# Optimization experiments

Measured on AMD Instinct MI355X. Metric: run time of the kernel, lower is better.

## Reference

```python
import jax, jax.numpy as jnp
import numpy as np

EPS = 1e-5
TOP_K = 2


def _dwconv3x3(x, w):
    # depthwise 3x3, stride 1, padding 1 (SAME)
    return jax.lax.conv_general_dilated(
        x, w, window_strides=(1, 1), padding='SAME',
        feature_group_count=x.shape[1],
        dimension_numbers=('NCHW', 'OIHW', 'NCHW'))


def _bn(x, g, b, m, v):
    # inference-mode BatchNorm2d
    s = g / jnp.sqrt(v + EPS)
    return x * s[None, :, None, None] + (b - m * s)[None, :, None, None]


def setup_inputs() -> dict:
    key = jax.random.key(0)
    ks = jax.random.split(key, 26)
    Bsz, D, H = 16, 384, 32
    S, E, HID = 64, 8, 768
    n, u = jax.random.normal, jax.random.uniform
    inp = {}
    inp['x'] = n(ks[0], (Bsz, D, H, H), jnp.float32)
    inp['dw1_w'] = n(ks[1], (D, 1, 3, 3)) * 0.1
    inp['bn1_g'] = u(ks[2], (D,), minval=0.5, maxval=1.5)
    inp['bn1_b'] = n(ks[3], (D,)) * 0.1
    inp['bn1_m'] = n(ks[4], (D,)) * 0.1
    inp['bn1_v'] = u(ks[5], (D,), minval=0.5, maxval=1.5)
    inp['dw2_w'] = n(ks[6], (D, 1, 3, 3)) * 0.1
    inp['bn2_g'] = u(ks[7], (D,), minval=0.5, maxval=1.5)
    inp['bn2_b'] = n(ks[8], (D,)) * 0.1
    inp['bn2_m'] = n(ks[9], (D,)) * 0.1
    inp['bn2_v'] = u(ks[10], (D,), minval=0.5, maxval=1.5)
    inp['ln_w'] = u(ks[11], (D,), minval=0.5, maxval=1.5)
    inp['ln_b'] = n(ks[12], (D,)) * 0.1
    inp['bcdt_w'] = n(ks[13], (3 * S, D)) * 0.02
    inp['dws_w'] = n(ks[14], (3 * S, 1, 3, 3)) * 0.1
    inp['hproj_w'] = n(ks[15], (D, D)) * 0.02
    inp['A'] = u(ks[16], (S,), minval=1.0, maxval=16.0)
    inp['gate_w'] = n(ks[17], (E, D)) * 0.02
    inp['gate_b'] = n(ks[18], (E,)) * 0.02
    inp['w1'] = n(ks[19], (E, HID, D)) * 0.02
    inp['b1'] = n(ks[20], (E, HID)) * 0.02
    inp['w2'] = n(ks[21], (E, D, HID)) * 0.02
    inp['b2'] = n(ks[22], (E, D)) * 0.02
    inp['w3'] = n(ks[23], (E, HID, D)) * 0.02
    inp['b3'] = n(ks[24], (E, HID)) * 0.02
    return inp


def reference(x, dw1_w, bn1_g, bn1_b, bn1_m, bn1_v, dw2_w, bn2_g, bn2_b, bn2_m,
              bn2_v, ln_w, ln_b, bcdt_w, dws_w, hproj_w, A, gate_w, gate_b,
              w1, b1, w2, b2, w3, b3):
    Bsz, D, H, W = x.shape
    L = H * W
    S = A.shape[0]
    E = gate_w.shape[0]
    # x = x + dwconv1(x)
    x = x + _bn(_dwconv3x3(x, dw1_w), bn1_g, bn1_b, bn1_m, bn1_v)
    x_prev = x
    # LayerNorm1D over channel dim of (B, C, L)
    xf = x.reshape(Bsz, D, L)
    mu = xf.mean(axis=1, keepdims=True)
    var = xf.var(axis=1, keepdims=True)
    xn = (xf - mu) / jnp.sqrt(var + EPS) * ln_w[None, :, None] + ln_b[None, :, None]
    # Slim_SSD mixer
    bcdt = jnp.einsum('cd,bdl->bcl', bcdt_w, xn)            # 1x1 conv1d
    bcdt = _dwconv3x3(bcdt.reshape(Bsz, 3 * S, H, W), dws_w).reshape(Bsz, 3 * S, L)
    Bm, Cm, dt = jnp.split(bcdt, 3, axis=1)                  # each (B, S, L)
    Am = jax.nn.softmax(dt + A[None, :, None], axis=-1)      # softmax over L
    h = jnp.einsum('bdl,bsl->bds', xn, Am * Bm)              # (B, D, S)
    h = jax.nn.silu(jnp.einsum('ed,bds->bes', hproj_w, h))   # h_proj + SiLU
    y = jnp.einsum('bes,bsl->bel', h, Cm).reshape(Bsz, D, H, W)
    x = x_prev + y
    # x = x + dwconv2(x)
    x = x + _bn(_dwconv3x3(x, dw2_w), bn2_g, bn2_b, bn2_m, bn2_v)
    # SparseMoE (TopkRouter, eval mode, filter_radio=0 -> mask==1, bias buffer==0)
    t = x.transpose(0, 2, 3, 1).reshape(-1, D)               # (N, D) tokens
    N = t.shape[0]
    logits = t @ gate_w.T + gate_b                           # (N, E)
    vals, idx = jax.lax.top_k(logits, TOP_K)
    probs = jax.nn.softmax(vals, axis=1)                     # softmax over top-k logits
    wfull = jnp.zeros((N, E), t.dtype).at[jnp.arange(N)[:, None], idx].set(probs)
    ymoe = jnp.zeros_like(t)
    for e in range(E):
        he = jax.nn.silu(t @ w1[e].T + b1[e]) * (t @ w3[e].T + b3[e])
        ymoe = ymoe + (he @ w2[e].T + b2[e]) * wfull[:, e:e + 1]
    x = x + ymoe.reshape(Bsz, H, W, D).transpose(0, 3, 1, 2)
    # dropout is identity in eval mode
    return (x, h)
```

## Files before the change

### kernel.cpp

```cpp
#include <hip/hip_runtime.h>
#include <hip/hip_bf16.h>

#define BSZ 16
#define DCH 384
#define LSP 1024
#define SST 64
#define NEXP 8
#define HID 768
#define NTOK 16384
#define MOE_MAXT 520

#define OFF_X1    0ULL
#define OFF_XN    25165824ULL
#define OFF_BCDT  50331648ULL
#define OFF_BCDTC 62914560ULL
#define OFF_H     75497472ULL
#define OFF_X2    77070336ULL
#define OFF_META  102236160ULL
#define OFF_LOGITS (OFF_META)
#define OFF_PROBS  (OFF_META +  524288ULL)
#define OFF_IDX    (OFF_META +  655360ULL)
#define OFF_CNT    (OFF_META +  786432ULL)
#define OFF_FILL   (OFF_META +  786464ULL)
#define OFF_OFFS   (OFF_META +  786496ULL)
#define OFF_TOFF   (OFF_META +  786560ULL)
#define OFF_LTOK   (OFF_META +  786624ULL)
#define OFF_LP     (OFF_META +  917696ULL)
#define OFF_TPOS   (OFF_META + 1048768ULL)
#define OFF_HE    0ULL
#define OFF_T16   OFF_BCDT
#define OFF_W1B   OFF_BCDTC
#define OFF_W3B   (OFF_BCDTC + 4718592ULL)
#define OFF_W2B   (OFF_BCDTC + 9437184ULL)
#define OFF_YMOE  OFF_X2
#define OFF_HPRE  OFF_X2

typedef __attribute__((ext_vector_type(8))) short bf16x8;
typedef __attribute__((ext_vector_type(4))) float f32x4;
typedef __attribute__((ext_vector_type(4))) unsigned short u16x4;

__device__ __forceinline__ unsigned short f2bf(float f) {
  union { float f; unsigned int u; } x; x.f = f;
  unsigned int r = (x.u + 0x7fffu + ((x.u >> 16) & 1u)) >> 16;
  return (unsigned short)r;
}
__device__ __forceinline__ float bf2f(unsigned short s) {
  union { unsigned int u; float f; } x; x.u = ((unsigned int)s) << 16; return x.f;
}

__device__ __forceinline__ void async16(const void* g, void* l) {
  unsigned long long gi = reinterpret_cast<unsigned long long>(g);
  unsigned int li = (unsigned int)reinterpret_cast<unsigned long long>(l);
  __builtin_amdgcn_global_load_lds(
      (const __attribute__((address_space(1))) unsigned int*)gi,
      (__attribute__((address_space(3))) unsigned int*)(unsigned long long)li,
      16, 0, 0);
}

__global__ void k_dwbnres(const float* __restrict__ x, const float* __restrict__ w,
                          const float* __restrict__ g, const float* __restrict__ bb,
                          const float* __restrict__ mm, const float* __restrict__ vv,
                          float* __restrict__ out, int C) {
  int bc = blockIdx.x;
  int c = bc % C;
  __shared__ float tile[34 * 34];
  const float* img = x + (size_t)bc * 1024;
  for (int i = threadIdx.x; i < 34 * 34; i += 256) tile[i] = 0.f;
  __syncthreads();
  for (int i = threadIdx.x; i < 1024; i += 256) {
    int r = i >> 5, cc = i & 31;
    tile[(r + 1) * 34 + (cc + 1)] = img[i];
  }
  __syncthreads();
  float w0 = w[c*9+0], w1 = w[c*9+1], w2 = w[c*9+2], w3 = w[c*9+3], w4 = w[c*9+4],
        w5 = w[c*9+5], w6 = w[c*9+6], w7 = w[c*9+7], w8 = w[c*9+8];
  bool res = (g != nullptr);
  float scale = 1.f, bias = 0.f;
  if (res) { float s = g[c] * rsqrtf(vv[c] + 1e-5f); scale = s; bias = bb[c] - mm[c] * s; }
  for (int i = threadIdx.x; i < 1024; i += 256) {
    int r = i >> 5, cc = i & 31;
    const float* t0 = &tile[r * 34 + cc];
    float acc = t0[0]*w0 + t0[1]*w1 + t0[2]*w2
              + t0[34]*w3 + t0[35]*w4 + t0[36]*w5
              + t0[68]*w6 + t0[69]*w7 + t0[70]*w8;
    float o = res ? (t0[35] + acc * scale + bias) : acc;
    out[(size_t)bc * 1024 + i] = o;
  }
}

__global__ void k_layernorm(const float* __restrict__ x, const float* __restrict__ lw,
                            const float* __restrict__ lb, float* __restrict__ xn) {
  int lane = threadIdx.x & 63;
  int slice = threadIdx.x >> 6;
  int pos0 = blockIdx.x * 64;
  int b = pos0 >> 10;
  int l = (pos0 & 1023) + lane;
  const float* xb = x + (size_t)b * DCH * LSP + l;
  float s = 0.f, s2 = 0.f;
  for (int d = slice * 96; d < slice * 96 + 96; d++) {
    float v = xb[(size_t)d * LSP];
    s += v; s2 += v * v;
  }
  __shared__ float red[2][4][64];
  red[0][slice][lane] = s; red[1][slice][lane] = s2;
  __syncthreads();
  if (slice == 0) {
    s  = red[0][0][lane] + red[0][1][lane] + red[0][2][lane] + red[0][3][lane];
    s2 = red[1][0][lane] + red[1][1][lane] + red[1][2][lane] + red[1][3][lane];
    float mu = s * (1.f / 384.f);
    float var = s2 * (1.f / 384.f) - mu * mu;
    red[0][0][lane] = mu;
    red[1][0][lane] = rsqrtf(var + 1e-5f);
  }
  __syncthreads();
  float mu = red[0][0][lane], rs = red[1][0][lane];
  float* xnb = xn + (size_t)b * DCH * LSP + l;
  for (int d = slice * 96; d < slice * 96 + 96; d++) {
    float v = xb[(size_t)d * LSP];
    xnb[(size_t)d * LSP] = (v - mu) * rs * lw[d] + lb[d];
  }
}

__global__ void k_bcdt(const float* __restrict__ xn, const float* __restrict__ wt,
                       float* __restrict__ out) {
  int lt = blockIdx.x, ct = blockIdx.y, b = blockIdx.z;
  __shared__ float wsm[64][33];
  __shared__ float xs[32][129];
  int lg = threadIdx.x & 31, cg = threadIdx.x >> 5;
  float acc[8][4];
  for (int i = 0; i < 8; i++) for (int j = 0; j < 4; j++) acc[i][j] = 0.f;
  const float* xb = xn + (size_t)b * DCH * LSP + lt * 128;
  for (int d0 = 0; d0 < 384; d0 += 32) {
    for (int i = threadIdx.x; i < 2048; i += 256) {
      int c = i >> 5, dd = i & 31;
      wsm[c][dd] = wt[(size_t)(ct * 64 + c) * 384 + d0 + dd];
    }
    for (int i = threadIdx.x; i < 4096; i += 256) {
      int dd = i >> 7, ll = i & 127;
      xs[dd][ll] = xb[(size_t)(d0 + dd) * LSP + ll];
    }
    __syncthreads();
    for (int dd = 0; dd < 32; dd++) {
      float xv[4];
      #pragma unroll
      for (int il = 0; il < 4; il++) xv[il] = xs[dd][lg + 32 * il];
      #pragma unroll
      for (int ic = 0; ic < 8; ic++) {
        float wv = wsm[cg + 8 * ic][dd];
        #pragma unroll
        for (int il = 0; il < 4; il++) acc[ic][il] += wv * xv[il];
      }
    }
    __syncthreads();
  }
  for (int ic = 0; ic < 8; ic++)
    for (int il = 0; il < 4; il++)
      out[(size_t)b * 196608 + (size_t)(ct * 64 + cg + 8 * ic) * 1024 + lt * 128 + lg + 32 * il] = acc[ic][il];
}

__global__ void k_softmax(float* __restrict__ bc, const float* __restrict__ Av) {
  int b = blockIdx.x >> 6, s = blockIdx.x & 63;
  float* row = bc + (size_t)b * 196608 + (size_t)(128 + s) * 1024;
  float a = Av[s];
  int t = threadIdx.x;
  float v[4]; float mx = -3.0e38f;
  #pragma unroll
  for (int i = 0; i < 4; i++) { v[i] = row[t + 256 * i] + a; mx = fmaxf(mx, v[i]); }
  #pragma unroll
  for (int off = 32; off >= 1; off >>= 1) mx = fmaxf(mx, __shfl_xor(mx, off));
  __shared__ float redm[4], reds[4];
  if ((t & 63) == 0) redm[t >> 6] = mx;
  __syncthreads();
  mx = fmaxf(fmaxf(redm[0], redm[1]), fmaxf(redm[2], redm[3]));
  float sm = 0.f;
  #pragma unroll
  for (int i = 0; i < 4; i++) { v[i] = __expf(v[i] - mx); sm += v[i]; }
  #pragma unroll
  for (int off = 32; off >= 1; off >>= 1) sm += __shfl_xor(sm, off);
  if ((t & 63) == 0) reds[t >> 6] = sm;
  __syncthreads();
  sm = reds[0] + reds[1] + reds[2] + reds[3];
  float inv = 1.f / sm;
  #pragma unroll
  for (int i = 0; i < 4; i++) row[t + 256 * i] = v[i] * inv;
}

__global__ void k_h(const float* __restrict__ xn, const float* __restrict__ bc,
                    float* __restrict__ h) {
  int dt_ = blockIdx.x, ls = blockIdx.y, b = blockIdx.z;
  __shared__ float xs[64][65];
  __shared__ float ab[64][65];
  int tid = threadIdx.x;
  int sg4 = tid & 15, dg4 = tid >> 4;
  float acc[4][4];
  #pragma unroll
  for (int i = 0; i < 4; i++)
    #pragma unroll
    for (int j = 0; j < 4; j++) acc[i][j] = 0.f;
  const float* Bm = bc + (size_t)b * 196608;
  const float* Am = Bm + 131072;
  const float* xb = xn + (size_t)b * DCH * LSP + (size_t)(dt_ * 64) * LSP;
  for (int l0 = ls * 128; l0 < ls * 128 + 128; l0 += 64) {
    for (int i = tid; i < 4096; i += 256) {
      int r = i >> 6, ll = i & 63;
      xs[r][ll] = xb[(size_t)r * LSP + l0 + ll];
      ab[r][ll] = Am[(size_t)r * 1024 + l0 + ll] * Bm[(size_t)r * 1024 + l0 + ll];
    }
    __syncthreads();
    for (int ll = 0; ll < 64; ll++) {
      float xv[4], av[4];
      #pragma unroll
      for (int i = 0; i < 4; i++) xv[i] = xs[dg4 * 4 + i][ll];
      #pragma unroll
      for (int j = 0; j < 4; j++) av[j] = ab[sg4 * 4 + j][ll];
      #pragma unroll
      for (int i = 0; i < 4; i++)
        #pragma unroll
        for (int j = 0; j < 4; j++) acc[i][j] += xv[i] * av[j];
    }
    __syncthreads();
  }
  float* hb = h + (size_t)b * DCH * SST + (size_t)(dt_ * 64) * 64;
  #pragma unroll
  for (int i = 0; i < 4; i++)
    #pragma unroll
    for (int j = 0; j < 4; j++)
      atomicAdd(&hb[(size_t)(dg4 * 4 + i) * 64 + sg4 * 4 + j], acc[i][j]);
}

__global__ void k_hproj(const float* __restrict__ h, const float* __restrict__ pw,
                        float* __restrict__ hpre) {
  int et = blockIdx.x, ks = blockIdx.y, b = blockIdx.z;
  __shared__ float hs[64][65];
  __shared__ float ps[64][65];
  int tid = threadIdx.x;
  int sg4 = tid & 15, eg4 = tid >> 4;
  float acc[4][4];
  #pragma unroll
  for (int i = 0; i < 4; i++)
    #pragma unroll
    for (int j = 0; j < 4; j++) acc[i][j] = 0.f;
  for (int d0 = ks * 128; d0 < ks * 128 + 128; d0 += 64) {
    for (int i = tid; i < 4096; i += 256) {
      int r = i >> 6, cc = i & 63;
      hs[r][cc] = h[(size_t)b * DCH * SST + (size_t)(d0 + r) * 64 + cc];
      ps[r][cc] = pw[(size_t)(et * 64 + r) * 384 + d0 + cc];
    }
    __syncthreads();
    for (int dd = 0; dd < 64; dd++) {
      float pv[4], hv[4];
      #pragma unroll
      for (int i = 0; i < 4; i++) pv[i] = ps[eg4 * 4 + i][dd];
      #pragma unroll
      for (int j = 0; j < 4; j++) hv[j] = hs[dd][sg4 * 4 + j];
      #pragma unroll
      for (int i = 0; i < 4; i++)
        #pragma unroll
        for (int j = 0; j < 4; j++) acc[i][j] += pv[i] * hv[j];
    }
    __syncthreads();
  }
  float* hb = hpre + (size_t)b * DCH * SST + (size_t)(et * 64) * 64;
  #pragma unroll
  for (int i = 0; i < 4; i++)
    #pragma unroll
    for (int j = 0; j < 4; j++)
      atomicAdd(&hb[(size_t)(eg4 * 4 + i) * 64 + sg4 * 4 + j], acc[i][j]);
}

__global__ void k_silu(const float* __restrict__ hpre, float* __restrict__ h2) {
  int i = blockIdx.x * 256 + threadIdx.x;
  float4 v = ((const float4*)hpre)[i];
  v.x = v.x / (1.f + __expf(-v.x));
  v.y = v.y / (1.f + __expf(-v.y));
  v.z = v.z / (1.f + __expf(-v.z));
  v.w = v.w / (1.f + __expf(-v.w));
  ((float4*)h2)[i] = v;
}

__global__ void k_y(const float* __restrict__ h2, const float* __restrict__ bc,
                    const float* __restrict__ x1, float* __restrict__ x2) {
  int lt = blockIdx.x, dt_ = blockIdx.y, b = blockIdx.z;
  __shared__ float hss[32][65];
  __shared__ float cs[64][129];
  int lg = threadIdx.x & 31, dg = threadIdx.x >> 5;
  float acc[4][4];
  for (int i = 0; i < 4; i++) for (int j = 0; j < 4; j++) acc[i][j] = 0.f;
  for (int i = threadIdx.x; i < 2048; i += 256) {
    int r = i >> 6, cc = i & 63;
    hss[r][cc] = h2[(size_t)b * DCH * SST + (size_t)(dt_ * 32 + r) * 64 + cc];
  }
  const float* Cm = bc + (size_t)b * 196608 + 65536;
  for (int i = threadIdx.x; i < 8192; i += 256) {
    int ss = i >> 7, ll = i & 127;
    cs[ss][ll] = Cm[(size_t)ss * 1024 + lt * 128 + ll];
  }
  __syncthreads();
  for (int ss = 0; ss < 64; ss++) {
    float cv[4];
    #pragma unroll
    for (int il = 0; il < 4; il++) cv[il] = cs[ss][lg + 32 * il];
    #pragma unroll
    for (int id = 0; id < 4; id++) {
      float hv = hss[dg * 4 + id][ss];
      #pragma unroll
      for (int il = 0; il < 4; il++) acc[id][il] += hv * cv[il];
    }
  }
  size_t base = (size_t)b * DCH * LSP + (size_t)(dt_ * 32) * LSP + lt * 128;
  for (int id = 0; id < 4; id++)
    for (int il = 0; il < 4; il++) {
      size_t o = base + (size_t)(dg * 4 + id) * LSP + lg + 32 * il;
      x2[o] = x1[o] + acc[id][il];
    }
}

__global__ void k_router(const float* __restrict__ x3, const float* __restrict__ gw,
                         const float* __restrict__ gb, float* __restrict__ logits) {
  __shared__ float xs[64][65];
  __shared__ float gs[8][64];
  int blk = blockIdx.x;
  int b = blk >> 4; int l0 = (blk & 15) * 64;
  int lg = threadIdx.x & 63, eg = threadIdx.x >> 6;
  float acc0 = 0.f, acc1 = 0.f;
  const float* xb = x3 + (size_t)b * DCH * LSP + l0;
  for (int d0 = 0; d0 < 384; d0 += 64) {
    for (int i = threadIdx.x; i < 4096; i += 256) {
      int dd = i >> 6, ll = i & 63;
      xs[dd][ll] = xb[(size_t)(d0 + dd) * LSP + ll];
    }
    for (int i = threadIdx.x; i < 512; i += 256) {
      int e = i >> 6, dd = i & 63;
      gs[e][dd] = gw[(size_t)e * 384 + d0 + dd];
    }
    __syncthreads();
    for (int dd = 0; dd < 64; dd++) {
      float xv = xs[dd][lg];
      acc0 += gs[eg][dd] * xv;
      acc1 += gs[eg + 4][dd] * xv;
    }
    __syncthreads();
  }
  int n = b * 1024 + l0 + lg;
  logits[(size_t)n * 8 + eg]     = acc0 + gb[eg];
  logits[(size_t)n * 8 + eg + 4] = acc1 + gb[eg + 4];
}

__global__ void k_topk(const float* __restrict__ logits, float* __restrict__ probs,
                       int* __restrict__ idx, int* __restrict__ cnt) {
  __shared__ int lcnt[8];
  if (threadIdx.x < 8) lcnt[threadIdx.x] = 0;
  __syncthreads();
  int n = blockIdx.x * 256 + threadIdx.x;
  float lv[8];
  for (int e = 0; e < 8; e++) lv[e] = logits[(size_t)n * 8 + e];
  int i1 = 0; float v1 = lv[0];
  for (int e = 1; e < 8; e++) if (lv[e] > v1) { v1 = lv[e]; i1 = e; }
  int i2 = -1; float v2 = -3.0e38f;
  for (int e = 0; e < 8; e++) { if (e == i1) continue; if (lv[e] > v2) { v2 = lv[e]; i2 = e; } }
  float p1 = 1.f / (1.f + __expf(v2 - v1));
  probs[n * 2] = p1; probs[n * 2 + 1] = 1.f - p1;
  idx[n * 2] = i1; idx[n * 2 + 1] = i2;
  atomicAdd(&lcnt[i1], 1); atomicAdd(&lcnt[i2], 1);
  __syncthreads();
  if (threadIdx.x < 8) atomicAdd(&cnt[threadIdx.x], lcnt[threadIdx.x]);
}

__global__ void k_offsets(const int* __restrict__ cnt, int* __restrict__ offs,
                          int* __restrict__ toff) {
  if (threadIdx.x == 0) {
    int a = 0, t = 0;
    for (int e = 0; e < 8; e++) {
      offs[e] = a; toff[e] = t;
      a += cnt[e]; t += (cnt[e] + 63) >> 6;
    }
    toff[8] = t;
  }
}

__global__ void k_build(const int* __restrict__ idx, const float* __restrict__ probs,
                        const int* __restrict__ offs, int* __restrict__ fill,
                        int* __restrict__ ltok, float* __restrict__ lp,
                        int* __restrict__ tpos) {
  __shared__ int lcnt[8], lbase[8];
  if (threadIdx.x < 8) lcnt[threadIdx.x] = 0;
  __syncthreads();
  int n = blockIdx.x * 256 + threadIdx.x;
  int e0 = idx[n * 2], e1 = idx[n * 2 + 1];
  int o0 = atomicAdd(&lcnt[e0], 1);
  int o1 = atomicAdd(&lcnt[e1], 1);
  __syncthreads();
  if (threadIdx.x < 8) lbase[threadIdx.x] = atomicAdd(&fill[threadIdx.x], lcnt[threadIdx.x]);
  __syncthreads();
  int p0 = offs[e0] + lbase[e0] + o0;
  int p1 = offs[e1] + lbase[e1] + o1;
  ltok[p0] = n; lp[p0] = probs[n * 2];     tpos[n * 2] = p0;
  ltok[p1] = n; lp[p1] = probs[n * 2 + 1]; tpos[n * 2 + 1] = p1;
}

__global__ void k_t16(const float* __restrict__ x3, unsigned short* __restrict__ t16) {
  __shared__ float tl[32][33];
  int lt = blockIdx.x, dt_ = blockIdx.y, b = blockIdx.z;
  const float* xb = x3 + (size_t)b * DCH * LSP + (size_t)(dt_ * 32) * LSP + lt * 32;
  for (int i = threadIdx.x; i < 1024; i += 256) {
    int dd = i >> 5, ll = i & 31;
    tl[dd][ll] = xb[(size_t)dd * LSP + ll];
  }
  __syncthreads();
  for (int i = threadIdx.x; i < 1024; i += 256) {
    int ll = i >> 5, dd = i & 31;
    int n = b * 1024 + lt * 32 + ll;
    t16[(size_t)n * 384 + dt_ * 32 + dd] = f2bf(tl[dd][ll]);
  }
}

__global__ void k_f2bf3(const float* __restrict__ s0, const float* __restrict__ s1,
                        const float* __restrict__ s2, unsigned short* __restrict__ d0,
                        unsigned short* __restrict__ d1, unsigned short* __restrict__ d2,
                        int n4) {
  int i = blockIdx.x * 256 + threadIdx.x;
  if (i >= n4) return;
  const float* s = (blockIdx.y == 0) ? s0 : (blockIdx.y == 1) ? s1 : s2;
  unsigned short* d = (blockIdx.y == 0) ? d0 : (blockIdx.y == 1) ? d1 : d2;
  float4 v = ((const float4*)s)[i];
  u16x4 o;
  o.x = f2bf(v.x); o.y = f2bf(v.y); o.z = f2bf(v.z); o.w = f2bf(v.w);
  ((u16x4*)d)[i] = o;
}

__global__ void __launch_bounds__(256) k_moe1(
    const unsigned short* __restrict__ t16, const unsigned short* __restrict__ w1,
    const unsigned short* __restrict__ w3, const float* __restrict__ b1,
    const float* __restrict__ b3, const int* __restrict__ ltok,
    const int* __restrict__ cnt, const int* __restrict__ offs,
    const int* __restrict__ toff, unsigned short* __restrict__ he) {
  int tb = blockIdx.x;
  if (tb >= toff[8]) return;
  int e = 0;
  #pragma unroll
  for (int i = 1; i < 8; i++) if (toff[i] <= tb) e = i;
  int rt = tb - toff[e];
  int ne = cnt[e], base = offs[e];
  int ct = blockIdx.y;
  __shared__ unsigned short As[64 * 64];
  __shared__ unsigned short B1s[128 * 64];
  __shared__ unsigned short B3s[128 * 64];
  __shared__ int toks[64];
  int tid = threadIdx.x;
  if (tid < 64) {
    int r = rt * 64 + tid;
    toks[tid] = ltok[base + (r < ne ? r : ne - 1)];
  }
  __syncthreads();
  int lane = tid & 63, wave = tid >> 6;
  int wm = (wave & 1) * 32, wn = (wave >> 1) * 64;
  int fm = lane & 15, fq = lane >> 4;
  int srow = lane >> 3, slot = lane & 7;
  f32x4 acc1[2][4], acc3[2][4];
  #pragma unroll
  for (int mi = 0; mi < 2; mi++)
    #pragma unroll
    for (int ni = 0; ni < 4; ni++) { acc1[mi][ni] = (f32x4)(0.f); acc3[mi][ni] = (f32x4)(0.f); }
  const unsigned short* w1e = w1 + ((size_t)e * 768 + ct * 128) * 384;
  const unsigned short* w3e = w3 + ((size_t)e * 768 + ct * 128) * 384;
  int ar0 = wave * 16 + srow, ar1 = wave * 16 + 8 + srow;
  const unsigned short* ag0 = t16 + (size_t)toks[ar0] * 384 + ((slot ^ (ar0 & 7)) * 8);
  const unsigned short* ag1 = t16 + (size_t)toks[ar1] * 384 + ((slot ^ (ar1 & 7)) * 8);
  const unsigned short* b1g[4]; const unsigned short* b3g[4];
  #pragma unroll
  for (int ii = 0; ii < 4; ii++) {
    int brow = wave * 32 + ii * 8 + srow;
    int coff = (slot ^ (brow & 7)) * 8;
    b1g[ii] = w1e + (size_t)brow * 384 + coff;
    b3g[ii] = w3e + (size_t)brow * 384 + coff;
  }
  unsigned short* asw0 = &As[(wave * 16) * 64];
  unsigned short* asw1 = &As[(wave * 16 + 8) * 64];
  for (int k0 = 0; k0 < 384; k0 += 64) {
    async16(ag0 + k0, asw0);
    async16(ag1 + k0, asw1);
    #pragma unroll
    for (int ii = 0; ii < 4; ii++) {
      async16(b1g[ii] + k0, &B1s[(wave * 32 + ii * 8) * 64]);
      async16(b3g[ii] + k0, &B3s[(wave * 32 + ii * 8) * 64]);
    }
    __syncthreads();
    #pragma unroll
    for (int kk = 0; kk < 2; kk++) {
      int c = kk * 4 + fq;
      bf16x8 av[2];
      #pragma unroll
      for (int mi = 0; mi < 2; mi++) {
        int row = wm + mi * 16 + fm;
        av[mi] = *(bf16x8*)&As[row * 64 + ((c ^ (row & 7)) * 8)];
      }
      #pragma unroll
      for (int ni = 0; ni < 4; ni++) {
        int row = wn + ni * 16 + fm;
        int off = row * 64 + ((c ^ (row & 7)) * 8);
        bf16x8 b1v = *(bf16x8*)&B1s[off];
        bf16x8 b3v = *(bf16x8*)&B3s[off];
        #pragma unroll
        for (int mi = 0; mi < 2; mi++) {
          acc1[mi][ni] = __builtin_amdgcn_mfma_f32_16x16x32_bf16(av[mi], b1v, acc1[mi][ni], 0, 0, 0);
          acc3[mi][ni] = __builtin_amdgcn_mfma_f32_16x16x32_bf16(av[mi], b3v, acc3[mi][ni], 0, 0, 0);
        }
      }
    }
    __syncthreads();
  }
  #pragma unroll
  for (int mi = 0; mi < 2; mi++)
    #pragma unroll
    for (int ni = 0; ni < 4; ni++)
      #pragma unroll
      for (int r = 0; r < 4; r++) {
        int lr = wm + mi * 16 + fq * 4 + r;
        int gr = rt * 64 + lr;
        if (gr < ne) {
          int col = ct * 128 + wn + ni * 16 + fm;
          float z1 = acc1[mi][ni][r] + b1[e * 768 + col];
          float z3 = acc3[mi][ni][r] + b3[e * 768 + col];
          float val = (z1 / (1.f + __expf(-z1))) * z3;
          he[((size_t)base + gr) * 768 + col] = f2bf(val);
        }
      }
}

__global__ void __launch_bounds__(256) k_moe2(
    const unsigned short* __restrict__ he, const unsigned short* __restrict__ w2,
    const float* __restrict__ b2, const float* __restrict__ lp,
    const int* __restrict__ cnt, const int* __restrict__ offs,
    const int* __restrict__ toff, unsigned short* __restrict__ ymoe) {
  int tb = blockIdx.x;
  if (tb >= toff[8]) return;
  int e = 0;
  #pragma unroll
  for (int i = 1; i < 8; i++) if (toff[i] <= tb) e = i;
  int rt = tb - toff[e];
  int ne = cnt[e], base = offs[e];
  int ct = blockIdx.y;
  __shared__ unsigned short As[64 * 64];
  __shared__ unsigned short Bs[128 * 64];
  __shared__ float lps[64];
  int tid = threadIdx.x;
  if (tid < 64) {
    int r = rt * 64 + tid;
    lps[tid] = lp[base + (r < ne ? r : ne - 1)];
  }
  int lane = tid & 63, wave = tid >> 6;
  int wm = (wave & 1) * 32, wn = (wave >> 1) * 64;
  int fm = lane & 15, fq = lane >> 4;
  int srow = lane >> 3, slot = lane & 7;
  f32x4 acc[2][4];
  #pragma unroll
  for (int mi = 0; mi < 2; mi++)
    #pragma unroll
    for (int ni = 0; ni < 4; ni++) acc[mi][ni] = (f32x4)(0.f);
  const unsigned short* w2e = w2 + ((size_t)e * 384 + ct * 128) * 768;
  int ar0 = wave * 16 + srow, ar1 = wave * 16 + 8 + srow;
  int g0 = base + rt * 64 + ar0; if (g0 > 32767) g0 = 32767;
  int g1 = base + rt * 64 + ar1; if (g1 > 32767) g1 = 32767;
  const unsigned short* ag0 = he + (size_t)g0 * 768 + ((slot ^ (ar0 & 7)) * 8);
  const unsigned short* ag1 = he + (size_t)g1 * 768 + ((slot ^ (ar1 & 7)) * 8);
  const unsigned short* bg[4];
  #pragma unroll
  for (int ii = 0; ii < 4; ii++) {
    int brow = wave * 32 + ii * 8 + srow;
    bg[ii] = w2e + (size_t)brow * 768 + ((slot ^ (brow & 7)) * 8);
  }
  unsigned short* asw0 = &As[(wave * 16) * 64];
  unsigned short* asw1 = &As[(wave * 16 + 8) * 64];
  for (int k0 = 0; k0 < 768; k0 += 64) {
    async16(ag0 + k0, asw0);
    async16(ag1 + k0, asw1);
    #pragma unroll
    for (int ii = 0; ii < 4; ii++)
      async16(bg[ii] + k0, &Bs[(wave * 32 + ii * 8) * 64]);
    __syncthreads();
    #pragma unroll
    for (int kk = 0; kk < 2; kk++) {
      int c = kk * 4 + fq;
      bf16x8 av[2];
      #pragma unroll
      for (int mi = 0; mi < 2; mi++) {
        int row = wm + mi * 16 + fm;
        av[mi] = *(bf16x8*)&As[row * 64 + ((c ^ (row & 7)) * 8)];
      }
      #pragma unroll
      for (int ni = 0; ni < 4; ni++) {
        int row = wn + ni * 16 + fm;
        bf16x8 bv = *(bf16x8*)&Bs[row * 64 + ((c ^ (row & 7)) * 8)];
        #pragma unroll
        for (int mi = 0; mi < 2; mi++)
          acc[mi][ni] = __builtin_amdgcn_mfma_f32_16x16x32_bf16(av[mi], bv, acc[mi][ni], 0, 0, 0);
      }
    }
    __syncthreads();
  }
  #pragma unroll
  for (int mi = 0; mi < 2; mi++)
    #pragma unroll
    for (int ni = 0; ni < 4; ni++)
      #pragma unroll
      for (int r = 0; r < 4; r++) {
        int lr = wm + mi * 16 + fq * 4 + r;
        int gr = rt * 64 + lr;
        if (gr < ne) {
          int col = ct * 128 + wn + ni * 16 + fm;
          float val = (acc[mi][ni][r] + b2[e * 384 + col]) * lps[lr];
          ymoe[((size_t)base + gr) * 384 + col] = f2bf(val);
        }
      }
}

__global__ void k_scatter(const unsigned short* __restrict__ ymoe,
                          const int* __restrict__ tpos, float* __restrict__ xout) {
  int dt_ = blockIdx.x;
  int lt = blockIdx.y;
  int b = blockIdx.z;
  int l = threadIdx.x & 63;
  int d0 = dt_ * 32 + (threadIdx.x >> 6) * 8;
  int n = b * 1024 + lt * 64 + l;
  int p0 = tpos[2 * n], p1 = tpos[2 * n + 1];
  bf16x8 y0 = *(const bf16x8*)(ymoe + (size_t)p0 * 384 + d0);
  bf16x8 y1 = *(const bf16x8*)(ymoe + (size_t)p1 * 384 + d0);
  size_t base = (size_t)b * DCH * LSP + (size_t)d0 * LSP + lt * 64 + l;
  #pragma unroll
  for (int k = 0; k < 8; k++) {
    float v = bf2f((unsigned short)y0[k]) + bf2f((unsigned short)y1[k]);
    xout[base + (size_t)k * LSP] += v;
  }
}

extern "C" void kernel_launch(void* const* d_in, const int* in_sizes, int n_in,
                              void* d_out, int out_size, void* d_ws, size_t ws_size,
                              hipStream_t stream) {
  const float* x      = (const float*)d_in[0];
  const float* dw1    = (const float*)d_in[1];
  const float* bn1g   = (const float*)d_in[2];
  const float* bn1b   = (const float*)d_in[3];
  const float* bn1m   = (const float*)d_in[4];
  const float* bn1v   = (const float*)d_in[5];
  const float* dw2    = (const float*)d_in[6];
  const float* bn2g   = (const float*)d_in[7];
  const float* bn2b   = (const float*)d_in[8];
  const float* bn2m   = (const float*)d_in[9];
  const float* bn2v   = (const float*)d_in[10];
  const float* lnw    = (const float*)d_in[11];
  const float* lnb    = (const float*)d_in[12];
  const float* bcdtw  = (const float*)d_in[13];
  const float* dwsw   = (const float*)d_in[14];
  const float* hprojw = (const float*)d_in[15];
  const float* Avec   = (const float*)d_in[16];
  const float* gatew  = (const float*)d_in[17];
  const float* gateb  = (const float*)d_in[18];
  const float* w1f    = (const float*)d_in[19];
  const float* b1f    = (const float*)d_in[20];
  const float* w2f    = (const float*)d_in[21];
  const float* b2f    = (const float*)d_in[22];
  const float* w3f    = (const float*)d_in[23];
  const float* b3f    = (const float*)d_in[24];

  char* wsb = (char*)d_ws;
  float* x1    = (float*)(wsb + OFF_X1);
  float* xn    = (float*)(wsb + OFF_XN);
  float* bcdt  = (float*)(wsb + OFF_BCDT);
  float* bcdtc = (float*)(wsb + OFF_BCDTC);
  float* hbuf  = (float*)(wsb + OFF_H);
  float* hpre  = (float*)(wsb + OFF_HPRE);
  float* x2    = (float*)(wsb + OFF_X2);
  float* logits = (float*)(wsb + OFF_LOGITS);
  float* probs  = (float*)(wsb + OFF_PROBS);
  int*   idx    = (int*)(wsb + OFF_IDX);
  int*   cnt    = (int*)(wsb + OFF_CNT);
  int*   fill   = (int*)(wsb + OFF_FILL);
  int*   offs   = (int*)(wsb + OFF_OFFS);
  int*   toff   = (int*)(wsb + OFF_TOFF);
  int*   ltok   = (int*)(wsb + OFF_LTOK);
  float* lp     = (float*)(wsb + OFF_LP);
  int*   tpos   = (int*)(wsb + OFF_TPOS);
  unsigned short* t16  = (unsigned short*)(wsb + OFF_T16);
  unsigned short* w1b  = (unsigned short*)(wsb + OFF_W1B);
  unsigned short* w3b  = (unsigned short*)(wsb + OFF_W3B);
  unsigned short* w2b  = (unsigned short*)(wsb + OFF_W2B);
  unsigned short* he   = (unsigned short*)(wsb + OFF_HE);
  unsigned short* ymoe = (unsigned short*)(wsb + OFF_YMOE);
  float* xout = (float*)d_out;
  float* h2   = xout + (size_t)BSZ * DCH * LSP;

  k_dwbnres<<<BSZ * DCH, 256, 0, stream>>>(x, dw1, bn1g, bn1b, bn1m, bn1v, x1, DCH);
  k_layernorm<<<NTOK / 64, 256, 0, stream>>>(x1, lnw, lnb, xn);
  k_bcdt<<<dim3(8, 3, BSZ), 256, 0, stream>>>(xn, bcdtw, bcdt);
  k_dwbnres<<<BSZ * 192, 256, 0, stream>>>(bcdt, dwsw, nullptr, nullptr, nullptr, nullptr, bcdtc, 192);
  k_softmax<<<BSZ * SST, 256, 0, stream>>>(bcdtc, Avec);
  hipMemsetAsync(hbuf, 0, (size_t)BSZ * DCH * SST * 4, stream);
  hipMemsetAsync(hpre, 0, (size_t)BSZ * DCH * SST * 4, stream);
  k_h<<<dim3(6, 8, BSZ), 256, 0, stream>>>(xn, bcdtc, hbuf);
  k_hproj<<<dim3(6, 3, BSZ), 256, 0, stream>>>(hbuf, hprojw, hpre);
  k_silu<<<(BSZ * DCH * SST / 4) / 256, 256, 0, stream>>>(hpre, h2);
  k_y<<<dim3(8, 12, BSZ), 256, 0, stream>>>(h2, bcdtc, x1, x2);
  k_dwbnres<<<BSZ * DCH, 256, 0, stream>>>(x2, dw2, bn2g, bn2b, bn2m, bn2v, xout, DCH);
  hipMemsetAsync(wsb + OFF_CNT, 0, 64, stream);
  k_router<<<256, 256, 0, stream>>>(xout, gatew, gateb, logits);
  k_topk<<<NTOK / 256, 256, 0, stream>>>(logits, probs, idx, cnt);
  k_offsets<<<1, 64, 0, stream>>>(cnt, offs, toff);
  k_build<<<NTOK / 256, 256, 0, stream>>>(idx, probs, offs, fill, ltok, lp, tpos);
  k_t16<<<dim3(32, 12, BSZ), 256, 0, stream>>>(xout, t16);
  int n4 = NEXP * HID * DCH / 4;
  k_f2bf3<<<dim3((n4 + 255) / 256, 3), 256, 0, stream>>>(w1f, w3f, w2f, w1b, w3b, w2b, n4);
  k_moe1<<<dim3(MOE_MAXT, 6), 256, 0, stream>>>(t16, w1b, w3b, b1f, b3f, ltok, cnt, offs, toff, he);
  k_moe2<<<dim3(MOE_MAXT, 3), 256, 0, stream>>>(he, w2b, b2f, lp, cnt, offs, toff, ymoe);
  k_scatter<<<dim3(12, 16, BSZ), 256, 0, stream>>>(ymoe, tpos, xout);
}
```

Before: 554.1 us.

## Run B/C/dt projection as bf16 MFMA GEMM on transposed normalized input

Replaces the fp32 scalar FMA tiled GEMM for the B/C/dt projection with a bf16 MFMA kernel. It adds async global-to-LDS loads with an XOR-swizzled shared layout. Two new preprocessing launches are added: one transposes the normalized activations to token-major bf16, and one converts the projection weights to bf16. This trades an extra pass over the 25MB activation, plus reduced precision, for much faster matrix math.

```diff
diff --git a/kernel.cpp b/kernel.cpp
--- a/kernel.cpp
+++ b/kernel.cpp
@@ -27,6 +27,7 @@
 #define OFF_LTOK   (OFF_META +  786624ULL)
 #define OFF_LP     (OFF_META +  917696ULL)
 #define OFF_TPOS   (OFF_META + 1048768ULL)
+#define OFF_WBC    (OFF_META + 1179840ULL)
 #define OFF_HE    0ULL
 #define OFF_T16   OFF_BCDT
 #define OFF_W1B   OFF_BCDTC
@@ -34,6 +35,7 @@
 #define OFF_W2B   (OFF_BCDTC + 9437184ULL)
 #define OFF_YMOE  OFF_X2
 #define OFF_HPRE  OFF_X2
+#define OFF_XNT   OFF_X2
 
 typedef __attribute__((ext_vector_type(8))) short bf16x8;
 typedef __attribute__((ext_vector_type(4))) float f32x4;
@@ -121,41 +123,73 @@
   }
 }
 
-__global__ void k_bcdt(const float* __restrict__ xn, const float* __restrict__ wt,
-                       float* __restrict__ out) {
+__global__ void __launch_bounds__(256) k_bcdt(
+    const unsigned short* __restrict__ xnT, const unsigned short* __restrict__ wbc,
+    float* __restrict__ out) {
   int lt = blockIdx.x, ct = blockIdx.y, b = blockIdx.z;
-  __shared__ float wsm[64][33];
-  __shared__ float xs[32][129];
-  int lg = threadIdx.x & 31, cg = threadIdx.x >> 5;
-  float acc[8][4];
-  for (int i = 0; i < 8; i++) for (int j = 0; j < 4; j++) acc[i][j] = 0.f;
-  const float* xb = xn + (size_t)b * DCH * LSP + lt * 128;
-  for (int d0 = 0; d0 < 384; d0 += 32) {
-    for (int i = threadIdx.x; i < 2048; i += 256) {
-      int c = i >> 5, dd = i & 31;
-      wsm[c][dd] = wt[(size_t)(ct * 64 + c) * 384 + d0 + dd];
-    }
-    for (int i = threadIdx.x; i < 4096; i += 256) {
-      int dd = i >> 7, ll = i & 127;
-      xs[dd][ll] = xb[(size_t)(d0 + dd) * LSP + ll];
-    }
-    __syncthreads();
-    for (int dd = 0; dd < 32; dd++) {
-      float xv[4];
-      #pragma unroll
-      for (int il = 0; il < 4; il++) xv[il] = xs[dd][lg + 32 * il];
-      #pragma unroll
-      for (int ic = 0; ic < 8; ic++) {
-        float wv = wsm[cg + 8 * ic][dd];
+  __shared__ unsigned short As[64 * 64];
+  __shared__ unsigned short Bs[128 * 64];
+  int tid = threadIdx.x;
+  int lane = tid & 63, wave = tid >> 6;
+  int wm = (wave & 1) * 32, wn = (wave >> 1) * 64;
+  int fm = lane & 15, fq = lane >> 4;
+  int srow = lane >> 3, slot = lane & 7;
+  f32x4 acc[2][4];
+  #pragma unroll
+  for (int mi = 0; mi < 2; mi++)
+    #pragma unroll
+    for (int ni = 0; ni < 4; ni++) acc[mi][ni] = (f32x4)(0.f);
+  const unsigned short* wge = wbc + (size_t)(ct * 64) * 384;
+  const unsigned short* xge = xnT + ((size_t)(b * 1024 + lt * 128)) * 384;
+  int ar0 = wave * 16 + srow, ar1 = ar0 + 8;
+  const unsigned short* ag0 = wge + (size_t)ar0 * 384 + ((slot ^ (ar0 & 7)) * 8);
+  const unsigned short* ag1 = wge + (size_t)ar1 * 384 + ((slot ^ (ar1 & 7)) * 8);
+  const unsigned short* bg[4];
+  #pragma unroll
+  for (int ii = 0; ii < 4; ii++) {
+    int brow = wave * 32 + ii * 8 + srow;
+    bg[ii] = xge + (size_t)brow * 384 + ((slot ^ (brow & 7)) * 8);
+  }
+  unsigned short* asw0 = &As[(wave * 16) * 64];
+  unsigned short* asw1 = &As[(wave * 16 + 8) * 64];
+  for (int k0 = 0; k0 < 384; k0 += 64) {
+    async16(ag0 + k0, asw0);
+    async16(ag1 + k0, asw1);
+    #pragma unroll
+    for (int ii = 0; ii < 4; ii++)
+      async16(bg[ii] + k0, &Bs[(wave * 32 + ii * 8) * 64]);
+    __syncthreads();
+    #pragma unroll
+    for (int kk = 0; kk < 2; kk++) {
+      int c = kk * 4 + fq;
+      bf16x8 av[2];
+      #pragma unroll
+      for (int mi = 0; mi < 2; mi++) {
+        int row = wm + mi * 16 + fm;
+        av[mi] = *(bf16x8*)&As[row * 64 + ((c ^ (row & 7)) * 8)];
+      }
+      #pragma unroll
+      for (int ni = 0; ni < 4; ni++) {
+        int row = wn + ni * 16 + fm;
+        bf16x8 bv = *(bf16x8*)&Bs[row * 64 + ((c ^ (row & 7)) * 8)];
         #pragma unroll
-        for (int il = 0; il < 4; il++) acc[ic][il] += wv * xv[il];
-      }
-    }
-    __syncthreads();
-  }
-  for (int ic = 0; ic < 8; ic++)
-    for (int il = 0; il < 4; il++)
-      out[(size_t)b * 196608 + (size_t)(ct * 64 + cg + 8 * ic) * 1024 + lt * 128 + lg + 32 * il] = acc[ic][il];
+        for (int mi = 0; mi < 2; mi++)
+          acc[mi][ni] = __builtin_amdgcn_mfma_f32_16x16x32_bf16(av[mi], bv, acc[mi][ni], 0, 0, 0);
+      }
+    }
+    __syncthreads();
+  }
+  float* ob = out + (size_t)b * 196608 + (size_t)(ct * 64) * 1024 + lt * 128;
+  #pragma unroll
+  for (int mi = 0; mi < 2; mi++)
+    #pragma unroll
+    for (int ni = 0; ni < 4; ni++)
+      #pragma unroll
+      for (int r = 0; r < 4; r++) {
+        int row = wm + mi * 16 + fq * 4 + r;
+        int col = wn + ni * 16 + fm;
+        ob[(size_t)row * 1024 + col] = acc[mi][ni][r];
+      }
 }
 
 __global__ void k_softmax(float* __restrict__ bc, const float* __restrict__ Av) {
@@ -412,6 +446,14 @@
     int n = b * 1024 + lt * 32 + ll;
     t16[(size_t)n * 384 + dt_ * 32 + dd] = f2bf(tl[dd][ll]);
   }
+}
+
+__global__ void k_wbf(const float* __restrict__ s, unsigned short* __restrict__ d) {
+  int i = blockIdx.x * 256 + threadIdx.x;
+  float4 v = ((const float4*)s)[i];
+  u16x4 o;
+  o.x = f2bf(v.x); o.y = f2bf(v.y); o.z = f2bf(v.z); o.w = f2bf(v.w);
+  ((u16x4*)d)[i] = o;
 }
 
 __global__ void k_f2bf3(const float* __restrict__ s0, const float* __restrict__ s1,
@@ -686,12 +728,16 @@
   unsigned short* w2b  = (unsigned short*)(wsb + OFF_W2B);
   unsigned short* he   = (unsigned short*)(wsb + OFF_HE);
   unsigned short* ymoe = (unsigned short*)(wsb + OFF_YMOE);
+  unsigned short* xnT  = (unsigned short*)(wsb + OFF_XNT);
+  unsigned short* wbc  = (unsigned short*)(wsb + OFF_WBC);
   float* xout = (float*)d_out;
   float* h2   = xout + (size_t)BSZ * DCH * LSP;
 
   k_dwbnres<<<BSZ * DCH, 256, 0, stream>>>(x, dw1, bn1g, bn1b, bn1m, bn1v, x1, DCH);
   k_layernorm<<<NTOK / 64, 256, 0, stream>>>(x1, lnw, lnb, xn);
-  k_bcdt<<<dim3(8, 3, BSZ), 256, 0, stream>>>(xn, bcdtw, bcdt);
+  k_t16<<<dim3(32, 12, BSZ), 256, 0, stream>>>(xn, xnT);
+  k_wbf<<<72, 256, 0, stream>>>(bcdtw, wbc);
+  k_bcdt<<<dim3(8, 3, BSZ), 256, 0, stream>>>(xnT, wbc, bcdt);
   k_dwbnres<<<BSZ * 192, 256, 0, stream>>>(bcdt, dwsw, nullptr, nullptr, nullptr, nullptr, bcdtc, 192);
   k_softmax<<<BSZ * SST, 256, 0, stream>>>(bcdtc, Avec);
   hipMemsetAsync(hbuf, 0, (size_t)BSZ * DCH * SST * 4, stream);
```

Result: faster. 505.6 us (-8.8%).
